# Kernel tuning notes

Hardware: AMD Instinct MI355X
Metric: run time of the kernel (lower is better)

## Reference

```python
import jax, jax.numpy as jnp
import numpy as np

B, S, T = 16384, 64, 64
I, M, H = 4, 16, 64  # input_dim, middle_dim, hidden_dim


def _cell(x, h, c, Wih, Whh, b):
    # PyTorch LSTM cell, gate order i, f, g, o; b = b_ih + b_hh
    gates = x @ Wih.T + h @ Whh.T + b
    i, f, g, o = jnp.split(gates, 4, axis=-1)
    c = jax.nn.sigmoid(f) * c + jax.nn.sigmoid(i) * jnp.tanh(g)
    h = jax.nn.sigmoid(o) * jnp.tanh(c)
    return h, c


def setup_inputs() -> dict:
    key = jax.random.key(0)
    ks = jax.random.split(key, 18)
    p = lambda k, shape: (jax.random.uniform(k, shape, jnp.float32) - 0.5) * 0.25
    return {
        "src": jax.random.normal(ks[0], (B, S, I), jnp.float32),
        "trg": jax.random.normal(ks[1], (B, T, I), jnp.float32),
        "W_in": p(ks[2], (M, I)), "b_in": p(ks[3], (M,)),
        "enc_Wih0": p(ks[4], (4 * H, M)), "enc_Whh0": p(ks[5], (4 * H, H)), "enc_b0": p(ks[6], (4 * H,)),
        "enc_Wih1": p(ks[7], (4 * H, H)), "enc_Whh1": p(ks[8], (4 * H, H)), "enc_b1": p(ks[9], (4 * H,)),
        "dec_Wih0": p(ks[10], (4 * H, M)), "dec_Whh0": p(ks[11], (4 * H, H)), "dec_b0": p(ks[12], (4 * H,)),
        "dec_Wih1": p(ks[13], (4 * H, H)), "dec_Whh1": p(ks[14], (4 * H, H)), "dec_b1": p(ks[15], (4 * H,)),
        "W_out": p(ks[16], (I, H)), "b_out": p(ks[17], (I,)),
    }


def reference(src, trg, W_in, b_in,
              enc_Wih0, enc_Whh0, enc_b0, enc_Wih1, enc_Whh1, enc_b1,
              dec_Wih0, dec_Whh0, dec_b0, dec_Wih1, dec_Whh1, dec_b1,
              W_out, b_out):
    b = src.shape[0]
    dt = src.dtype

    def layer_scan(xs, Wih, Whh, bb):
        # xs: [S, B, D] -> ys: [S, B, H], final (h, c)
        h0 = jnp.zeros((b, H), dt)
        def step(carry, x):
            h, c = carry
            h, c = _cell(x, h, c, Wih, Whh, bb)
            return (h, c), h
        (h, c), ys = jax.lax.scan(step, (h0, h0), xs)
        return ys, h, c

    # encoder: fc_in then 2-layer LSTM (dropout inactive in eval)
    mid = src @ W_in.T + b_in                      # [B, S, M]
    ys1, h1, c1 = layer_scan(mid.transpose(1, 0, 2), enc_Wih0, enc_Whh0, enc_b0)
    _, h2, c2 = layer_scan(ys1, enc_Wih1, enc_Whh1, enc_b1)

    # stepwise decoder, teacher_forcing_ratio=0 branch: next input = pred + trg[:, t-1]
    def dec_step(carry, trg_t):
        h1, c1, h2, c2, x = carry
        m = x @ W_in.T + b_in                      # [B, M]
        h1, c1 = _cell(m, h1, c1, dec_Wih0, dec_Whh0, dec_b0)
        h2, c2 = _cell(h1, h2, c2, dec_Wih1, dec_Whh1, dec_b1)
        pred = h2 @ W_out.T + b_out                # [B, I]
        return (h1, c1, h2, c2, pred + trg_t), pred

    init = (h1, c1, h2, c2, trg[:, 0])
    _, preds = jax.lax.scan(dec_step, init, trg.transpose(1, 0, 2))  # [T, B, I]
    return preds.transpose(1, 0, 2) + trg
```

## Files before the change

kernel.cpp:

```cpp
#include <hip/hip_runtime.h>

typedef __bf16 bf16x8 __attribute__((ext_vector_type(8)));
typedef float  f32x4  __attribute__((ext_vector_type(4)));

__device__ __forceinline__ unsigned short f2bf(float x){
  return __builtin_bit_cast(unsigned short, (__bf16)x);
}

__device__ __forceinline__ void bar_lds(){
  asm volatile("s_waitcnt lgkmcnt(0)" ::: "memory");
  __builtin_amdgcn_s_barrier();
  asm volatile("" ::: "memory");
}

__global__ void pack_weights(const float* __restrict__ eWih0, const float* __restrict__ eWhh0,
                             const float* __restrict__ eWih1, const float* __restrict__ eWhh1,
                             const float* __restrict__ dWih0, const float* __restrict__ dWhh0,
                             const float* __restrict__ dWih1, const float* __restrict__ dWhh1,
                             const float* __restrict__ Wout,
                             unsigned short* __restrict__ out){
  int t = blockIdx.x * 256 + threadIdx.x;
  if (t >= 226 * 64) return;
  int lane = t & 63;
  int f    = t >> 6;
  unsigned short vals[8];
  if (f >= 224){
    int kt = f - 224, n = lane & 15;
#pragma unroll
    for (int jj = 0; jj < 8; jj++){
      int k = kt * 32 + (lane >> 4) * 8 + jj;
      vals[jj] = (n < 4) ? f2bf(Wout[n * 64 + k]) : (unsigned short)0;
    }
  } else {
    const float *Wih, *Whh; int kx, ntile, kt;
    if (f < 48)       { Wih=eWih0; Whh=eWhh0; kx=16; ntile=f/3;        kt=f%3; }
    else if (f < 112) { Wih=eWih1; Whh=eWhh1; kx=64; ntile=(f-48)/4;   kt=(f-48)%4; }
    else if (f < 160) { Wih=dWih0; Whh=dWhh0; kx=16; ntile=(f-112)/3;  kt=(f-112)%3; }
    else              { Wih=dWih1; Whh=dWhh1; kx=64; ntile=(f-160)/4;  kt=(f-160)%4; }
    int n    = ntile * 16 + (lane & 15);
    int hoff = (kx == 16) ? 32 : 64;
    float scale = ((ntile >> 2) == 2) ? -2.88539008f : -1.44269504f;
#pragma unroll
    for (int jj = 0; jj < 8; jj++){
      int k = kt * 32 + (lane >> 4) * 8 + jj;
      float v;
      if (k < kx)        v = Wih[n * kx + k];
      else if (k < hoff) v = 0.0f;
      else               v = Whh[n * 64 + (k - hoff)];
      vals[jj] = f2bf(v * scale);
    }
  }
  uint4 o;
  o.x = (unsigned)vals[0] | ((unsigned)vals[1] << 16);
  o.y = (unsigned)vals[2] | ((unsigned)vals[3] << 16);
  o.z = (unsigned)vals[4] | ((unsigned)vals[5] << 16);
  o.w = (unsigned)vals[6] | ((unsigned)vals[7] << 16);
  ((uint4*)out)[f * 64 + lane] = o;
}

__device__ __forceinline__ void write_h(unsigned short* buf, int k, int quad,
                                        const unsigned short* h){
  unsigned short* p = buf + (((k >> 5) * 64) + quad * 4 + (((k >> 3) & 3) << 4)) * 8 + (k & 7);
#pragma unroll
  for (int e = 0; e < 4; e++) p[e * 8] = h[e];
}

__device__ __forceinline__ void load_frags(const unsigned short* __restrict__ pw,
                                           int base0, int base1, int w, int lane,
                                           bf16x8 (&B0)[3][4], bf16x8 (&B1)[4][4]){
#pragma unroll
  for (int g = 0; g < 4; g++){
    int nt = 4 * g + w;
#pragma unroll
    for (int kt = 0; kt < 3; kt++)
      B0[kt][g] = *(const bf16x8*)(pw + (((long)(base0 + nt * 3 + kt)) * 64 + lane) * 8);
#pragma unroll
    for (int kt = 0; kt < 4; kt++)
      B1[kt][g] = *(const bf16x8*)(pw + (((long)(base1 + nt * 4 + kt)) * 64 + lane) * 8);
  }
}

template<int KT, int SZ>
__device__ __forceinline__ void cell_compute(const unsigned short* __restrict__ A,
                                             const bf16x8 (&B)[KT][4],
                                             const float (&bias)[4],
                                             float (&c)[8],
                                             unsigned short (&hout)[8],
                                             int lane){
  f32x4 acc[4][2];
#pragma unroll
  for (int g = 0; g < 4; g++){
    f32x4 b = {bias[g], bias[g], bias[g], bias[g]};
    acc[g][0] = b; acc[g][1] = b;
  }
#pragma unroll
  for (int kt = 0; kt < KT; kt++){
    bf16x8 a0 = *(const bf16x8*)(A +      (kt * 64 + lane) * 8);
    bf16x8 a1 = *(const bf16x8*)(A + SZ + (kt * 64 + lane) * 8);
#pragma unroll
    for (int g = 0; g < 4; g++){
      acc[g][0] = __builtin_amdgcn_mfma_f32_16x16x32_bf16(a0, B[kt][g], acc[g][0], 0, 0, 0);
      acc[g][1] = __builtin_amdgcn_mfma_f32_16x16x32_bf16(a1, B[kt][g], acc[g][1], 0, 0, 0);
    }
  }
#pragma unroll
  for (int rt = 0; rt < 2; rt++){
#pragma unroll
    for (int e = 0; e < 4; e++){
      int idx = rt * 4 + e;
      float ei = __builtin_amdgcn_exp2f(acc[0][rt][e]);
      float ef = __builtin_amdgcn_exp2f(acc[1][rt][e]);
      float eg = __builtin_amdgcn_exp2f(acc[2][rt][e]);
      float eo = __builtin_amdgcn_exp2f(acc[3][rt][e]);
      float pf   = 1.0f + ef;
      float pig  = (1.0f + ei) * (1.0f + eg);
      float rden = __builtin_amdgcn_rcpf(pf * pig);
      float num  = fmaf(fmaf(-2.88539008f, eg, 2.88539008f), pf, c[idx] * pig);
      float c2   = num * rden;
      c[idx] = c2;
      float ec  = __builtin_amdgcn_exp2f(c2);
      float rot = __builtin_amdgcn_rcpf((1.0f + eo) * (1.0f + ec));
      hout[idx] = f2bf((ec - 1.0f) * rot);
    }
  }
}

__global__ __launch_bounds__(256, 2)
void lstm_main(const float* __restrict__ src, const float* __restrict__ trg,
               const float* __restrict__ W_in, const float* __restrict__ b_in,
               const float* __restrict__ eb0, const float* __restrict__ eb1,
               const float* __restrict__ db0, const float* __restrict__ db1,
               const float* __restrict__ bout,
               const unsigned short* __restrict__ pw,
               float* __restrict__ out){
  __shared__ __align__(16) unsigned short A0[2][2][1536];
  __shared__ __align__(16) unsigned short A1[2][2][2048];
  __shared__ __align__(16) float xsrc[2][128];
  __shared__ __align__(16) unsigned short sWoutF[1024];
  __shared__ __align__(16) unsigned short sWinF[512];

  const int tid  = threadIdx.x;
  const int lane = tid & 63;
  const int w    = tid >> 6;
  const int quad = lane >> 4;
  const int l16  = lane & 15;
  const int j    = 16 * w + l16;
  const int rowg0 = blockIdx.x * 32;
  const int mm   = tid & 15;
  const int xr   = tid >> 4;

  {
    uint4 z; z.x = z.y = z.z = z.w = 0u;
    uint4* a0p = (uint4*)A0;
    uint4* a1p = (uint4*)A1;
    for (int i = tid; i < 768;  i += 256) a0p[i] = z;
    for (int i = tid; i < 1024; i += 256) a1p[i] = z;
    if (tid < 128) ((uint4*)sWoutF)[tid] = ((const uint4*)pw)[224 * 64 + tid];
    if (tid < 64){
      unsigned short v[8] = {0,0,0,0,0,0,0,0};
      if (tid < 16){
#pragma unroll
        for (int jj = 0; jj < 4; jj++) v[jj] = f2bf(W_in[tid * 4 + jj]);
      }
      uint4 o;
      o.x = (unsigned)v[0] | ((unsigned)v[1] << 16);
      o.y = (unsigned)v[2] | ((unsigned)v[3] << 16);
      o.z = o.w = 0u;
      ((uint4*)sWinF)[tid] = o;
    }
    if (tid < 128) xsrc[0][tid] = src[(long)(rowg0 + (tid >> 2)) * 256 + (tid & 3)];
  }
  const float4 wv = *(const float4*)&W_in[mm * 4];
  const float  bin = b_in[mm];

  bf16x8 B0[3][4], B1[4][4];
  float bias0[4], bias1[4];
  float c0[8] = {0,0,0,0,0,0,0,0}, c1[8] = {0,0,0,0,0,0,0,0};
  load_frags(pw, 0, 48, w, lane, B0, B1);
#pragma unroll
  for (int g = 0; g < 4; g++){
    int n = 64*g + j;
    float s = (g == 2) ? -2.88539008f : -1.44269504f;
    bias0[g] = eb0[n] * s; bias1[g] = eb1[n] * s;
  }
  bar_lds();

  unsigned short h0r[8], h1r[8];
  const int xoff = (xr | ((mm >> 3) << 4)) * 8 + (mm & 7);

  for (int t = 0; t < 64; t++){
    int cur = t & 1, nxt = cur ^ 1;
    float xv;
    if (tid < 128)
      xv = src[(long)(rowg0 + (tid >> 2)) * 256 + ((t == 63 ? 63 : t + 1) << 2) + (tid & 3)];
    {
      float4 x0 = *(const float4*)&xsrc[cur][xr * 4];
      float4 x1 = *(const float4*)&xsrc[cur][(xr + 16) * 4];
      float m0 = bin + x0.x*wv.x + x0.y*wv.y + x0.z*wv.z + x0.w*wv.w;
      float m1 = bin + x1.x*wv.x + x1.y*wv.y + x1.z*wv.z + x1.w*wv.w;
      A0[cur][0][xoff] = f2bf(m0);
      A0[cur][1][xoff] = f2bf(m1);
    }
    if (tid < 128) xsrc[nxt][tid] = xv;
    bar_lds();
    cell_compute<3, 1536>(&A0[cur][0][0], B0, bias0, c0, h0r, lane);
#pragma unroll
    for (int rt = 0; rt < 2; rt++){
      write_h(&A0[nxt][rt][0], 32 + j, quad, h0r + rt * 4);
      write_h(&A1[cur][rt][0],      j, quad, h0r + rt * 4);
    }
    if (t > 0){
      cell_compute<4, 2048>(&A1[nxt][0][0], B1, bias1, c1, h1r, lane);
#pragma unroll
      for (int rt = 0; rt < 2; rt++)
        write_h(&A1[cur][rt][0], 64 + j, quad, h1r + rt * 4);
    }
  }
  bar_lds();
  cell_compute<4, 2048>(&A1[1][0][0], B1, bias1, c1, h1r, lane);
#pragma unroll
  for (int rt = 0; rt < 2; rt++)
    write_h(&A1[0][rt][0], 64 + j, quad, h1r + rt * 4);

  load_frags(pw, 112, 160, w, lane, B0, B1);
#pragma unroll
  for (int g = 0; g < 4; g++){
    int n = 64*g + j;
    float s = (g == 2) ? -2.88539008f : -1.44269504f;
    bias0[g] = db0[n] * s; bias1[g] = db1[n] * s;
  }
  const float4 bq   = *(const float4*)&b_in[quad * 4];
  f32x4 boT = {0.0f, 0.0f, 0.0f, 0.0f};
  if (quad == 0){
    float4 b4 = *(const float4*)bout;
    boT[0] = b4.x; boT[1] = b4.y; boT[2] = b4.z; boT[3] = b4.w;
  }
  {
    float4 x0 = *(const float4*)&trg[(long)(rowg0 + xr) * 256];
    float4 x1 = *(const float4*)&trg[(long)(rowg0 + xr + 16) * 256];
    float m0 = bin + x0.x*wv.x + x0.y*wv.y + x0.z*wv.z + x0.w*wv.w;
    float m1 = bin + x1.x*wv.x + x1.y*wv.y + x1.z*wv.z + x1.w*wv.w;
    A0[0][0][xoff] = f2bf(m0);
    A0[0][1][xoff] = f2bf(m1);
  }
  bar_lds();

  for (int t = 0; t < 64; t++){
    int cur = t & 1, nxt = cur ^ 1;
    float4 tpreT = {0.0f, 0.0f, 0.0f, 0.0f};
    if (w < 2 && quad == 0)
      tpreT = *(const float4*)&trg[(long)(rowg0 + w * 16 + l16) * 256 + t * 4];
    cell_compute<3, 1536>(&A0[cur][0][0], B0, bias0, c0, h0r, lane);
#pragma unroll
    for (int rt = 0; rt < 2; rt++){
      write_h(&A0[nxt][rt][0], 32 + j, quad, h0r + rt * 4);
      write_h(&A1[cur][rt][0],      j, quad, h0r + rt * 4);
    }
    bar_lds();
    cell_compute<4, 2048>(&A1[cur][0][0], B1, bias1, c1, h1r, lane);
#pragma unroll
    for (int rt = 0; rt < 2; rt++)
      write_h(&A1[nxt][rt][0], 64 + j, quad, h1r + rt * 4);
    bar_lds();
    if (w < 2){
      const unsigned short* Ah = &A1[nxt][w][0];
      bf16x8 hb0 = *(const bf16x8*)(Ah + (2 * 64 + lane) * 8);
      bf16x8 hb1 = *(const bf16x8*)(Ah + (3 * 64 + lane) * 8);
      bf16x8 wa0 = *(const bf16x8*)(sWoutF + lane * 8);
      bf16x8 wa1 = *(const bf16x8*)(sWoutF + 512 + lane * 8);
      f32x4 po = boT;
      po = __builtin_amdgcn_mfma_f32_16x16x32_bf16(wa0, hb0, po, 0, 0, 0);
      po = __builtin_amdgcn_mfma_f32_16x16x32_bf16(wa1, hb1, po, 0, 0, 0);
      unsigned int xp0 = 0u, xp1 = 0u;
      if (quad == 0){
        float4 xv;
        xv.x = po[0] + tpreT.x;  xv.y = po[1] + tpreT.y;
        xv.z = po[2] + tpreT.z;  xv.w = po[3] + tpreT.w;
        *(float4*)&out[(long)(rowg0 + w * 16 + l16) * 256 + t * 4] = xv;
        xp0 = (unsigned)f2bf(xv.x) | ((unsigned)f2bf(xv.y) << 16);
        xp1 = (unsigned)f2bf(xv.z) | ((unsigned)f2bf(xv.w) << 16);
      }
      uint4 xb_u; xb_u.x = xp0; xb_u.y = xp1; xb_u.z = 0u; xb_u.w = 0u;
      bf16x8 xb = __builtin_bit_cast(bf16x8, xb_u);
      bf16x8 wi = *(const bf16x8*)(sWinF + lane * 8);
      f32x4 pm = {bq.x, bq.y, bq.z, bq.w};
      pm = __builtin_amdgcn_mfma_f32_16x16x32_bf16(wi, xb, pm, 0, 0, 0);
      unsigned int mp0 = (unsigned)f2bf(pm[0]) | ((unsigned)f2bf(pm[1]) << 16);
      unsigned int mp1 = (unsigned)f2bf(pm[2]) | ((unsigned)f2bf(pm[3]) << 16);
      uint2 mw; mw.x = mp0; mw.y = mp1;
      *(uint2*)&A0[nxt][w][(l16 | ((quad >> 1) << 4)) * 8 + (quad & 1) * 4] = mw;
    }
    bar_lds();
  }
}

extern "C" void kernel_launch(void* const* d_in, const int* in_sizes, int n_in,
                              void* d_out, int out_size, void* d_ws, size_t ws_size,
                              hipStream_t stream){
  (void)n_in; (void)out_size; (void)ws_size;
  const float* src   = (const float*)d_in[0];
  const float* trg   = (const float*)d_in[1];
  const float* W_in  = (const float*)d_in[2];
  const float* b_in  = (const float*)d_in[3];
  const float* eWih0 = (const float*)d_in[4];
  const float* eWhh0 = (const float*)d_in[5];
  const float* eb0   = (const float*)d_in[6];
  const float* eWih1 = (const float*)d_in[7];
  const float* eWhh1 = (const float*)d_in[8];
  const float* eb1   = (const float*)d_in[9];
  const float* dWih0 = (const float*)d_in[10];
  const float* dWhh0 = (const float*)d_in[11];
  const float* db0   = (const float*)d_in[12];
  const float* dWih1 = (const float*)d_in[13];
  const float* dWhh1 = (const float*)d_in[14];
  const float* db1   = (const float*)d_in[15];
  const float* Wout  = (const float*)d_in[16];
  const float* bout  = (const float*)d_in[17];
  unsigned short* pw = (unsigned short*)d_ws;

  pack_weights<<<57, 256, 0, stream>>>(eWih0, eWhh0, eWih1, eWhh1,
                                       dWih0, dWhh0, dWih1, dWhh1, Wout, pw);

  int B    = in_sizes[0] / 256;
  int nblk = B / 32;
  lstm_main<<<nblk, 256, 0, stream>>>(src, trg, W_in, b_in, eb0, eb1, db0, db1,
                                      bout, pw, (float*)d_out);
}
```

Baseline: 440.6 us.

## Split decoder layer-0 GEMM to prefetch recurrent-h part before output projection

Splits the decoder layer-0 cell matmul into a start phase over the h0-dependent K tiles (kt=1,2), which is issued right after the layer-1 barrier, and a finish phase that adds the input-dependent K tile (kt=0) once the next x is written. This overlaps part of the layer-0 MFMA work with the output projection and feedback path on the serial critical chain. In exchange the accumulator array is live across the loop body, which raises register pressure under the 2-blocks-per-SM launch bound. It also depends on kt=1,2 of A0[nxt] already being valid at that point.

```diff
diff --git a/kernel.cpp b/kernel.cpp
--- a/kernel.cpp
+++ b/kernel.cpp
@@ -80,29 +80,8 @@
   }
 }
 
-template<int KT, int SZ>
-__device__ __forceinline__ void cell_compute(const unsigned short* __restrict__ A,
-                                             const bf16x8 (&B)[KT][4],
-                                             const float (&bias)[4],
-                                             float (&c)[8],
-                                             unsigned short (&hout)[8],
-                                             int lane){
-  f32x4 acc[4][2];
-#pragma unroll
-  for (int g = 0; g < 4; g++){
-    f32x4 b = {bias[g], bias[g], bias[g], bias[g]};
-    acc[g][0] = b; acc[g][1] = b;
-  }
-#pragma unroll
-  for (int kt = 0; kt < KT; kt++){
-    bf16x8 a0 = *(const bf16x8*)(A +      (kt * 64 + lane) * 8);
-    bf16x8 a1 = *(const bf16x8*)(A + SZ + (kt * 64 + lane) * 8);
-#pragma unroll
-    for (int g = 0; g < 4; g++){
-      acc[g][0] = __builtin_amdgcn_mfma_f32_16x16x32_bf16(a0, B[kt][g], acc[g][0], 0, 0, 0);
-      acc[g][1] = __builtin_amdgcn_mfma_f32_16x16x32_bf16(a1, B[kt][g], acc[g][1], 0, 0, 0);
-    }
-  }
+__device__ __forceinline__ void cell_act(f32x4 (&acc)[4][2], float (&c)[8],
+                                         unsigned short (&hout)[8]){
 #pragma unroll
   for (int rt = 0; rt < 2; rt++){
 #pragma unroll
@@ -125,6 +104,70 @@
   }
 }
 
+template<int KT, int SZ>
+__device__ __forceinline__ void cell_compute(const unsigned short* __restrict__ A,
+                                             const bf16x8 (&B)[KT][4],
+                                             const float (&bias)[4],
+                                             float (&c)[8],
+                                             unsigned short (&hout)[8],
+                                             int lane){
+  f32x4 acc[4][2];
+#pragma unroll
+  for (int g = 0; g < 4; g++){
+    f32x4 b = {bias[g], bias[g], bias[g], bias[g]};
+    acc[g][0] = b; acc[g][1] = b;
+  }
+#pragma unroll
+  for (int kt = 0; kt < KT; kt++){
+    bf16x8 a0 = *(const bf16x8*)(A +      (kt * 64 + lane) * 8);
+    bf16x8 a1 = *(const bf16x8*)(A + SZ + (kt * 64 + lane) * 8);
+#pragma unroll
+    for (int g = 0; g < 4; g++){
+      acc[g][0] = __builtin_amdgcn_mfma_f32_16x16x32_bf16(a0, B[kt][g], acc[g][0], 0, 0, 0);
+      acc[g][1] = __builtin_amdgcn_mfma_f32_16x16x32_bf16(a1, B[kt][g], acc[g][1], 0, 0, 0);
+    }
+  }
+  cell_act(acc, c, hout);
+}
+
+__device__ __forceinline__ void cell0_start(const unsigned short* __restrict__ A,
+                                            const bf16x8 (&B)[3][4],
+                                            const float (&bias)[4],
+                                            f32x4 (&acc)[4][2],
+                                            int lane){
+#pragma unroll
+  for (int g = 0; g < 4; g++){
+    f32x4 b = {bias[g], bias[g], bias[g], bias[g]};
+    acc[g][0] = b; acc[g][1] = b;
+  }
+#pragma unroll
+  for (int kt = 1; kt < 3; kt++){
+    bf16x8 a0 = *(const bf16x8*)(A +        (kt * 64 + lane) * 8);
+    bf16x8 a1 = *(const bf16x8*)(A + 1536 + (kt * 64 + lane) * 8);
+#pragma unroll
+    for (int g = 0; g < 4; g++){
+      acc[g][0] = __builtin_amdgcn_mfma_f32_16x16x32_bf16(a0, B[kt][g], acc[g][0], 0, 0, 0);
+      acc[g][1] = __builtin_amdgcn_mfma_f32_16x16x32_bf16(a1, B[kt][g], acc[g][1], 0, 0, 0);
+    }
+  }
+}
+
+__device__ __forceinline__ void cell0_finish(const unsigned short* __restrict__ A,
+                                             const bf16x8 (&B)[3][4],
+                                             f32x4 (&acc)[4][2],
+                                             float (&c)[8],
+                                             unsigned short (&hout)[8],
+                                             int lane){
+  bf16x8 a0 = *(const bf16x8*)(A +        lane * 8);
+  bf16x8 a1 = *(const bf16x8*)(A + 1536 + lane * 8);
+#pragma unroll
+  for (int g = 0; g < 4; g++){
+    acc[g][0] = __builtin_amdgcn_mfma_f32_16x16x32_bf16(a0, B[0][g], acc[g][0], 0, 0, 0);
+    acc[g][1] = __builtin_amdgcn_mfma_f32_16x16x32_bf16(a1, B[0][g], acc[g][1], 0, 0, 0);
+  }
+  cell_act(acc, c, hout);
+}
+
 __global__ __launch_bounds__(256, 2)
 void lstm_main(const float* __restrict__ src, const float* __restrict__ trg,
                const float* __restrict__ W_in, const float* __restrict__ b_in,
@@ -245,12 +288,15 @@
   }
   bar_lds();
 
+  f32x4 accP[4][2];
+  cell0_start(&A0[0][0][0], B0, bias0, accP, lane);
+
   for (int t = 0; t < 64; t++){
     int cur = t & 1, nxt = cur ^ 1;
     float4 tpreT = {0.0f, 0.0f, 0.0f, 0.0f};
     if (w < 2 && quad == 0)
       tpreT = *(const float4*)&trg[(long)(rowg0 + w * 16 + l16) * 256 + t * 4];
-    cell_compute<3, 1536>(&A0[cur][0][0], B0, bias0, c0, h0r, lane);
+    cell0_finish(&A0[cur][0][0], B0, accP, c0, h0r, lane);
 #pragma unroll
     for (int rt = 0; rt < 2; rt++){
       write_h(&A0[nxt][rt][0], 32 + j, quad, h0r + rt * 4);
@@ -262,6 +308,7 @@
     for (int rt = 0; rt < 2; rt++)
       write_h(&A1[nxt][rt][0], 64 + j, quad, h1r + rt * 4);
     bar_lds();
+    cell0_start(&A0[nxt][0][0], B0, bias0, accP, lane);
     if (w < 2){
       const unsigned short* Ah = &A1[nxt][w][0];
       bf16x8 hb0 = *(const bf16x8*)(Ah + (2 * 64 + lane) * 8);
```

Result: no change. 434.7 us (-1.3%).

## Split LSTM layers across separate waves with 512-thread blocks and partial precompute

Applied to the files above, without the earlier changes.

Doubles the block to 512 threads, so waves 0-3 own layer 0 and waves 4-7 own layer 1, each holding only its own weight fragments in registers. In the decoder, the matmul parts whose inputs are already known (layer0 K-tiles 1-2 for the next step, layer1 h-part K-tiles 2-3) run before the barrier, overlapping them with the other layer's work. This is meant to cut per-wave register pressure and serial work per timestep, raising occupancy and overlap. It adds inter-wave dependence through LDS and more complex barrier choreography.

```diff
diff --git a/kernel.cpp b/kernel.cpp
--- a/kernel.cpp
+++ b/kernel.cpp
@@ -65,44 +65,26 @@
   for (int e = 0; e < 4; e++) p[e * 8] = h[e];
 }
 
-__device__ __forceinline__ void load_frags(const unsigned short* __restrict__ pw,
-                                           int base0, int base1, int w, int lane,
-                                           bf16x8 (&B0)[3][4], bf16x8 (&B1)[4][4]){
-#pragma unroll
-  for (int g = 0; g < 4; g++){
-    int nt = 4 * g + w;
-#pragma unroll
-    for (int kt = 0; kt < 3; kt++)
-      B0[kt][g] = *(const bf16x8*)(pw + (((long)(base0 + nt * 3 + kt)) * 64 + lane) * 8);
-#pragma unroll
-    for (int kt = 0; kt < 4; kt++)
-      B1[kt][g] = *(const bf16x8*)(pw + (((long)(base1 + nt * 4 + kt)) * 64 + lane) * 8);
-  }
-}
-
-template<int KT, int SZ>
-__device__ __forceinline__ void cell_compute(const unsigned short* __restrict__ A,
-                                             const bf16x8 (&B)[KT][4],
-                                             const float (&bias)[4],
-                                             float (&c)[8],
-                                             unsigned short (&hout)[8],
-                                             int lane){
-  f32x4 acc[4][2];
-#pragma unroll
-  for (int g = 0; g < 4; g++){
-    f32x4 b = {bias[g], bias[g], bias[g], bias[g]};
-    acc[g][0] = b; acc[g][1] = b;
-  }
-#pragma unroll
-  for (int kt = 0; kt < KT; kt++){
-    bf16x8 a0 = *(const bf16x8*)(A +      (kt * 64 + lane) * 8);
-    bf16x8 a1 = *(const bf16x8*)(A + SZ + (kt * 64 + lane) * 8);
-#pragma unroll
-    for (int g = 0; g < 4; g++){
-      acc[g][0] = __builtin_amdgcn_mfma_f32_16x16x32_bf16(a0, B[kt][g], acc[g][0], 0, 0, 0);
-      acc[g][1] = __builtin_amdgcn_mfma_f32_16x16x32_bf16(a1, B[kt][g], acc[g][1], 0, 0, 0);
-    }
-  }
+__device__ __forceinline__ void load_bw(const unsigned short* __restrict__ pw,
+                                        bool isW0, int w4, int lane,
+                                        int base0, int base1, bf16x8 (&BW)[4][4]){
+  if (isW0){
+#pragma unroll
+    for (int g = 0; g < 4; g++)
+#pragma unroll
+      for (int kt = 0; kt < 3; kt++)
+        BW[g][kt] = *(const bf16x8*)(pw + (((long)(base0 + (4*g + w4)*3 + kt)) * 64 + lane) * 8);
+  } else {
+#pragma unroll
+    for (int g = 0; g < 4; g++)
+#pragma unroll
+      for (int kt = 0; kt < 4; kt++)
+        BW[g][kt] = *(const bf16x8*)(pw + (((long)(base1 + (4*g + w4)*4 + kt)) * 64 + lane) * 8);
+  }
+}
+
+__device__ __forceinline__ void cell_act(f32x4 (&acc)[4][2], float (&c)[8],
+                                         unsigned short (&hout)[8]){
 #pragma unroll
   for (int rt = 0; rt < 2; rt++){
 #pragma unroll
@@ -125,7 +107,35 @@
   }
 }
 
-__global__ __launch_bounds__(256, 2)
+template<int KT_LO, int KT_HI, int SZ, bool INIT, bool ACT>
+__device__ __forceinline__ void cell_part(const unsigned short* __restrict__ A,
+                                          const bf16x8 (&BW)[4][4],
+                                          const float (&bias)[4],
+                                          f32x4 (&acc)[4][2],
+                                          float (&c)[8],
+                                          unsigned short (&hout)[8],
+                                          int lane){
+  if constexpr (INIT){
+#pragma unroll
+    for (int g = 0; g < 4; g++){
+      f32x4 b = {bias[g], bias[g], bias[g], bias[g]};
+      acc[g][0] = b; acc[g][1] = b;
+    }
+  }
+#pragma unroll
+  for (int kt = KT_LO; kt < KT_HI; kt++){
+    bf16x8 a0 = *(const bf16x8*)(A +      (kt * 64 + lane) * 8);
+    bf16x8 a1 = *(const bf16x8*)(A + SZ + (kt * 64 + lane) * 8);
+#pragma unroll
+    for (int g = 0; g < 4; g++){
+      acc[g][0] = __builtin_amdgcn_mfma_f32_16x16x32_bf16(a0, BW[g][kt], acc[g][0], 0, 0, 0);
+      acc[g][1] = __builtin_amdgcn_mfma_f32_16x16x32_bf16(a1, BW[g][kt], acc[g][1], 0, 0, 0);
+    }
+  }
+  if constexpr (ACT) cell_act(acc, c, hout);
+}
+
+__global__ __launch_bounds__(512, 4)
 void lstm_main(const float* __restrict__ src, const float* __restrict__ trg,
                const float* __restrict__ W_in, const float* __restrict__ b_in,
                const float* __restrict__ eb0, const float* __restrict__ eb1,
@@ -142,25 +152,27 @@
   const int tid  = threadIdx.x;
   const int lane = tid & 63;
   const int w    = tid >> 6;
+  const int w4   = w & 3;
+  const bool isW0 = (w < 4);
   const int quad = lane >> 4;
   const int l16  = lane & 15;
-  const int j    = 16 * w + l16;
+  const int jj   = 16 * w4 + l16;
   const int rowg0 = blockIdx.x * 32;
   const int mm   = tid & 15;
-  const int xr   = tid >> 4;
+  const int xr   = (tid >> 4) & 15;
 
   {
     uint4 z; z.x = z.y = z.z = z.w = 0u;
     uint4* a0p = (uint4*)A0;
     uint4* a1p = (uint4*)A1;
-    for (int i = tid; i < 768;  i += 256) a0p[i] = z;
-    for (int i = tid; i < 1024; i += 256) a1p[i] = z;
+    for (int i = tid; i < 768;  i += 512) a0p[i] = z;
+    for (int i = tid; i < 1024; i += 512) a1p[i] = z;
     if (tid < 128) ((uint4*)sWoutF)[tid] = ((const uint4*)pw)[224 * 64 + tid];
     if (tid < 64){
       unsigned short v[8] = {0,0,0,0,0,0,0,0};
       if (tid < 16){
 #pragma unroll
-        for (int jj = 0; jj < 4; jj++) v[jj] = f2bf(W_in[tid * 4 + jj]);
+        for (int q = 0; q < 4; q++) v[q] = f2bf(W_in[tid * 4 + q]);
       }
       uint4 o;
       o.x = (unsigned)v[0] | ((unsigned)v[1] << 16);
@@ -173,19 +185,21 @@
   const float4 wv = *(const float4*)&W_in[mm * 4];
   const float  bin = b_in[mm];
 
-  bf16x8 B0[3][4], B1[4][4];
-  float bias0[4], bias1[4];
-  float c0[8] = {0,0,0,0,0,0,0,0}, c1[8] = {0,0,0,0,0,0,0,0};
-  load_frags(pw, 0, 48, w, lane, B0, B1);
+  bf16x8 BW[4][4];
+  float bias[4];
+  f32x4 acc[4][2];
+  float cc[8] = {0,0,0,0,0,0,0,0};
+  unsigned short hr[8];
+
+  load_bw(pw, isW0, w4, lane, 0, 48, BW);
 #pragma unroll
   for (int g = 0; g < 4; g++){
-    int n = 64*g + j;
+    int n = 64*g + jj;
     float s = (g == 2) ? -2.88539008f : -1.44269504f;
-    bias0[g] = eb0[n] * s; bias1[g] = eb1[n] * s;
+    bias[g] = (isW0 ? eb0[n] : eb1[n]) * s;
   }
   bar_lds();
 
-  unsigned short h0r[8], h1r[8];
   const int xoff = (xr | ((mm >> 3) << 4)) * 8 + (mm & 7);
 
   for (int t = 0; t < 64; t++){
@@ -193,7 +207,7 @@
     float xv;
     if (tid < 128)
       xv = src[(long)(rowg0 + (tid >> 2)) * 256 + ((t == 63 ? 63 : t + 1) << 2) + (tid & 3)];
-    {
+    if (tid < 256){
       float4 x0 = *(const float4*)&xsrc[cur][xr * 4];
       float4 x1 = *(const float4*)&xsrc[cur][(xr + 16) * 4];
       float m0 = bin + x0.x*wv.x + x0.y*wv.y + x0.z*wv.z + x0.w*wv.w;
@@ -203,39 +217,41 @@
     }
     if (tid < 128) xsrc[nxt][tid] = xv;
     bar_lds();
-    cell_compute<3, 1536>(&A0[cur][0][0], B0, bias0, c0, h0r, lane);
-#pragma unroll
-    for (int rt = 0; rt < 2; rt++){
-      write_h(&A0[nxt][rt][0], 32 + j, quad, h0r + rt * 4);
-      write_h(&A1[cur][rt][0],      j, quad, h0r + rt * 4);
-    }
-    if (t > 0){
-      cell_compute<4, 2048>(&A1[nxt][0][0], B1, bias1, c1, h1r, lane);
+    if (isW0){
+      cell_part<0, 3, 1536, true, true>(&A0[cur][0][0], BW, bias, acc, cc, hr, lane);
+#pragma unroll
+      for (int rt = 0; rt < 2; rt++){
+        write_h(&A0[nxt][rt][0], 32 + jj, quad, hr + rt * 4);
+        write_h(&A1[cur][rt][0],      jj, quad, hr + rt * 4);
+      }
+    } else if (t > 0){
+      cell_part<0, 4, 2048, true, true>(&A1[nxt][0][0], BW, bias, acc, cc, hr, lane);
 #pragma unroll
       for (int rt = 0; rt < 2; rt++)
-        write_h(&A1[cur][rt][0], 64 + j, quad, h1r + rt * 4);
+        write_h(&A1[cur][rt][0], 64 + jj, quad, hr + rt * 4);
     }
   }
   bar_lds();
-  cell_compute<4, 2048>(&A1[1][0][0], B1, bias1, c1, h1r, lane);
-#pragma unroll
-  for (int rt = 0; rt < 2; rt++)
-    write_h(&A1[0][rt][0], 64 + j, quad, h1r + rt * 4);
-
-  load_frags(pw, 112, 160, w, lane, B0, B1);
+  if (!isW0){
+    cell_part<0, 4, 2048, true, true>(&A1[1][0][0], BW, bias, acc, cc, hr, lane);
+#pragma unroll
+    for (int rt = 0; rt < 2; rt++)
+      write_h(&A1[0][rt][0], 64 + jj, quad, hr + rt * 4);
+  }
+  load_bw(pw, isW0, w4, lane, 112, 160, BW);
 #pragma unroll
   for (int g = 0; g < 4; g++){
-    int n = 64*g + j;
+    int n = 64*g + jj;
     float s = (g == 2) ? -2.88539008f : -1.44269504f;
-    bias0[g] = db0[n] * s; bias1[g] = db1[n] * s;
-  }
-  const float4 bq   = *(const float4*)&b_in[quad * 4];
+    bias[g] = (isW0 ? db0[n] : db1[n]) * s;
+  }
+  const float4 bq = *(const float4*)&b_in[quad * 4];
   f32x4 boT = {0.0f, 0.0f, 0.0f, 0.0f};
   if (quad == 0){
     float4 b4 = *(const float4*)bout;
     boT[0] = b4.x; boT[1] = b4.y; boT[2] = b4.z; boT[3] = b4.w;
   }
-  {
+  if (tid < 256){
     float4 x0 = *(const float4*)&trg[(long)(rowg0 + xr) * 256];
     float4 x1 = *(const float4*)&trg[(long)(rowg0 + xr + 16) * 256];
     float m0 = bin + x0.x*wv.x + x0.y*wv.y + x0.z*wv.z + x0.w*wv.w;
@@ -243,26 +259,36 @@
     A0[0][0][xoff] = f2bf(m0);
     A0[0][1][xoff] = f2bf(m1);
   }
+  if (isW0)
+    cell_part<1, 3, 1536, true, false>(&A0[0][0][0], BW, bias, acc, cc, hr, lane);
   bar_lds();
 
   for (int t = 0; t < 64; t++){
     int cur = t & 1, nxt = cur ^ 1;
     float4 tpreT = {0.0f, 0.0f, 0.0f, 0.0f};
-    if (w < 2 && quad == 0)
-      tpreT = *(const float4*)&trg[(long)(rowg0 + w * 16 + l16) * 256 + t * 4];
-    cell_compute<3, 1536>(&A0[cur][0][0], B0, bias0, c0, h0r, lane);
-#pragma unroll
-    for (int rt = 0; rt < 2; rt++){
-      write_h(&A0[nxt][rt][0], 32 + j, quad, h0r + rt * 4);
-      write_h(&A1[cur][rt][0],      j, quad, h0r + rt * 4);
+    if (isW0){
+      if (w < 2 && quad == 0)
+        tpreT = *(const float4*)&trg[(long)(rowg0 + w * 16 + l16) * 256 + t * 4];
+      cell_part<0, 1, 1536, false, true>(&A0[cur][0][0], BW, bias, acc, cc, hr, lane);
+#pragma unroll
+      for (int rt = 0; rt < 2; rt++){
+        write_h(&A0[nxt][rt][0], 32 + jj, quad, hr + rt * 4);
+        write_h(&A1[cur][rt][0],      jj, quad, hr + rt * 4);
+      }
+    } else {
+      cell_part<2, 4, 2048, true, false>(&A1[cur][0][0], BW, bias, acc, cc, hr, lane);
     }
     bar_lds();
-    cell_compute<4, 2048>(&A1[cur][0][0], B1, bias1, c1, h1r, lane);
-#pragma unroll
-    for (int rt = 0; rt < 2; rt++)
-      write_h(&A1[nxt][rt][0], 64 + j, quad, h1r + rt * 4);
+    if (isW0){
+      cell_part<1, 3, 1536, true, false>(&A0[nxt][0][0], BW, bias, acc, cc, hr, lane);
+    } else {
+      cell_part<0, 2, 2048, false, true>(&A1[cur][0][0], BW, bias, acc, cc, hr, lane);
+#pragma unroll
+      for (int rt = 0; rt < 2; rt++)
+        write_h(&A1[nxt][rt][0], 64 + jj, quad, hr + rt * 4);
+    }
     bar_lds();
-    if (w < 2){
+    if (isW0 && w < 2){
       const unsigned short* Ah = &A1[nxt][w][0];
       bf16x8 hb0 = *(const bf16x8*)(Ah + (2 * 64 + lane) * 8);
       bf16x8 hb1 = *(const bf16x8*)(Ah + (3 * 64 + lane) * 8);
@@ -323,6 +349,6 @@
 
   int B    = in_sizes[0] / 256;
   int nblk = B / 32;
-  lstm_main<<<nblk, 256, 0, stream>>>(src, trg, W_in, b_in, eb0, eb1, db0, db1,
+  lstm_main<<<nblk, 512, 0, stream>>>(src, trg, W_in, b_in, eb0, eb1, db0, db1,
                                       bout, pw, (float*)d_out);
 }
```

Result: slower. 886.7 us (+101.3%).
